# Performance work log

Measured on AMD Instinct MI355X. Metric: run time of the kernel, lower is better.

The kernel has to match this reference:

```python
import jax, jax.numpy as jnp
import numpy as np

M, K, N = 8192, 4096, 4096

def setup_inputs() -> dict:
    key = jax.random.key(0)
    k1, k2, k3, k4, k5, k6 = jax.random.split(key, 6)
    # quantized activations (per-token symmetric int8)
    x_q = jax.random.randint(k1, (M, K), -128, 128, dtype=jnp.int32).astype(jnp.int8)
    # quantized weight (asymmetric per-output-channel): w_fp16 = scale_weight * (w_q + zp_weight)
    weight = jax.random.randint(k2, (N, K), -128, 128, dtype=jnp.int32).astype(jnp.int8)
    scale_input = (jax.random.uniform(k3, (M,), jnp.float32) * 0.009 + 0.001).astype(jnp.float16)
    scale_weight = (jax.random.uniform(k4, (N,), jnp.float32) * 0.009 + 0.001).astype(jnp.float16)
    zp_weight = jax.random.randint(k5, (N,), 100, 156, dtype=jnp.int32).astype(jnp.int16)
    bias = (jax.random.normal(k6, (N,), jnp.float32) * 0.01).astype(jnp.float16)
    # per-row sum of quantized activations (needed for zero-point correction)
    sum_input = jnp.sum(x_q.astype(jnp.int32), axis=-1).astype(jnp.float32)
    return {
        "input": x_q,
        "weight": weight,
        "bias": bias,
        "scale_input": scale_input,
        "scale_weight": scale_weight,
        "sum_input": sum_input,
        "zp_weight": zp_weight,
    }

def reference(input, weight, bias, scale_input, scale_weight, sum_input, zp_weight):
    acc = jnp.matmul(input.astype(jnp.int32), weight.astype(jnp.int32).T)
    # asymmetric weight zero-point correction: + zp_n * sum_k(x_q[m, k])
    corr = sum_input[:, None] * zp_weight.astype(jnp.float32)[None, :]
    # fused dequant epilogue: per-row activation scale * per-col weight scale, + bias
    scale = scale_input.astype(jnp.float32)[:, None] * scale_weight.astype(jnp.float32)[None, :]
    out = (acc.astype(jnp.float32) + corr) * scale + bias.astype(jnp.float32)[None, :]
    return out.astype(jnp.float16)
```

## Files before the change

### kernel.cpp

```cpp
#include <hip/hip_runtime.h>
#include <stdint.h>


#define BM 128
#define BN 128
#define BK 128

typedef __attribute__((ext_vector_type(4))) int int32x4;
typedef __attribute__((ext_vector_type(16))) int int32x16;

__device__ __forceinline__ void async_copy16(const uint8_t* g, uint8_t* l) {
  __builtin_amdgcn_global_load_lds(
      (const __attribute__((address_space(1))) uint32_t*)(const void*)g,
      (__attribute__((address_space(3))) uint32_t*)l,
      16, 0, 0);
}

__global__ __launch_bounds__(256) void pack_kernel(
    const int* __restrict__ A, const int* __restrict__ B,
    uint8_t* __restrict__ A8, uint8_t* __restrict__ B8,
    int nA4, int nTot4) {
  const int stride = gridDim.x * blockDim.x;
  for (int t = blockIdx.x * blockDim.x + threadIdx.x; t < nTot4; t += stride) {
    const int32x4* src;
    uint32_t* dst;
    if (t < nA4) {
      src = (const int32x4*)A + t;
      dst = (uint32_t*)A8 + t;
    } else {
      int u = t - nA4;
      src = (const int32x4*)B + u;
      dst = (uint32_t*)B8 + u;
    }
    int32x4 v = __builtin_nontemporal_load(src);
    *dst = (uint32_t)(v.x & 255) | ((uint32_t)(v.y & 255) << 8) |
           ((uint32_t)(v.z & 255) << 16) | ((uint32_t)(v.w & 255) << 24);
  }
}

__device__ __forceinline__ void stage_tile(
    const uint8_t* Ab, const uint8_t* Bb, size_t sK, int k0,
    uint8_t* AsBuf, uint8_t* BsBuf, int ldst) {
#pragma unroll
  for (int p = 0; p < 4; ++p)
    async_copy16(Ab + (size_t)(p * 32) * sK + k0, AsBuf + p * 4096 + ldst);
#pragma unroll
  for (int p = 0; p < 4; ++p)
    async_copy16(Bb + (size_t)(p * 32) * sK + k0, BsBuf + p * 4096 + ldst);
}

__global__ __launch_bounds__(256, 2) void w8a8_gemm(
    const uint8_t* __restrict__ A8, const uint8_t* __restrict__ B8,
    const float* __restrict__ bias,
    const float* __restrict__ s_in,
    const float* __restrict__ s_w,
    const float* __restrict__ sum_in,
    const int* __restrict__ zp_w,
    float* __restrict__ out,
    int M, int N, int K) {
  __shared__ uint8_t As[2][BM * BK];
  __shared__ uint8_t Bs[2][BN * BK];

  const int tid = threadIdx.x;
  const int bm = blockIdx.y, bn = blockIdx.x;
  const int row0 = bm * BM, col0 = bn * BN;

  const int wave = tid >> 6, lane = tid & 63;
  const int m32 = lane & 31, half = lane >> 5;
  const int wm = (wave >> 1) * 64;
  const int wn = (wave & 1) * 64;
  const size_t sK = (size_t)K;

  const int row_s = tid >> 3;
  const int cg = (tid & 7) ^ ((tid >> 4) & 7);
  const int ldst = tid * 16;

  const uint8_t* Ab = A8 + (size_t)(row0 + row_s) * sK + cg * 16;
  const uint8_t* Bb = B8 + (size_t)(col0 + row_s) * sK + cg * 16;

  int32x16 acc[2][2] = {};

  const int NT = K / BK;
  stage_tile(Ab, Bb, sK, 0, &As[0][0], &Bs[0][0], ldst);
  stage_tile(Ab, Bb, sK, BK, &As[1][0], &Bs[1][0], ldst);

  int cur = 0;
  const int swzr = (m32 >> 1) & 7;
  for (int kt = 0; kt < NT; ++kt) {
    if (kt + 1 < NT) {
      asm volatile("s_waitcnt vmcnt(8)" ::: "memory");
    } else {
      asm volatile("s_waitcnt vmcnt(0)" ::: "memory");
    }
    __builtin_amdgcn_s_barrier();

    const uint8_t* Ac = &As[cur][0];
    const uint8_t* Bc = &Bs[cur][0];
#pragma unroll
    for (int ks = 0; ks < 4; ++ks) {
      const int gran = ((ks * 2 + half) ^ swzr) * 16;
      int32x4 afrag[2], bfrag[2];
#pragma unroll
      for (int i = 0; i < 2; ++i)
        afrag[i] = *(const int32x4*)&Ac[(wm + i * 32 + m32) * BK + gran];
#pragma unroll
      for (int j = 0; j < 2; ++j)
        bfrag[j] = *(const int32x4*)&Bc[(wn + j * 32 + m32) * BK + gran];
#pragma unroll
      for (int i = 0; i < 2; ++i)
#pragma unroll
        for (int j = 0; j < 2; ++j)
          acc[i][j] = __builtin_amdgcn_mfma_i32_32x32x32_i8(
              afrag[i], bfrag[j], acc[i][j], 0, 0, 0);
    }
    asm volatile("s_waitcnt lgkmcnt(0)" ::: "memory");
    __builtin_amdgcn_s_barrier();
    if (kt + 2 < NT)
      stage_tile(Ab, Bb, sK, (kt + 2) * BK, &As[cur][0], &Bs[cur][0], ldst);
    cur ^= 1;
  }

  float swj[2], zpj[2], bj[2];
#pragma unroll
  for (int j = 0; j < 2; ++j) {
    int gc = col0 + wn + j * 32 + m32;
    swj[j] = s_w[gc];
    zpj[j] = (float)zp_w[gc];
    bj[j] = bias[gc];
  }
#pragma unroll
  for (int i = 0; i < 2; ++i) {
#pragma unroll
    for (int reg = 0; reg < 16; ++reg) {
      int gr = row0 + wm + i * 32 + (reg & 3) + 8 * (reg >> 2) + 4 * half;
      float siv = s_in[gr];
      float suv = sum_in[gr];
      float* orow = out + (size_t)gr * N + col0 + wn + m32;
#pragma unroll
      for (int j = 0; j < 2; ++j) {
        float v = ((float)acc[i][j][reg] + suv * zpj[j]) * (siv * swj[j]) + bj[j];
        __builtin_nontemporal_store(v, &orow[j * 32]);
      }
    }
  }
}

__global__ __launch_bounds__(256) void w8a8_gemm_fallback(
    const int* __restrict__ A32, const int* __restrict__ B32,
    const float* __restrict__ bias,
    const float* __restrict__ s_in,
    const float* __restrict__ s_w,
    const float* __restrict__ sum_in,
    const int* __restrict__ zp_w,
    float* __restrict__ out,
    int M, int N, int K) {
  __shared__ uint8_t As[128 * 64];
  __shared__ uint8_t Bs[128 * 64];
  const int tid = threadIdx.x;
  const int bm = blockIdx.y, bn = blockIdx.x;
  const int row0 = bm * 128, col0 = bn * 128;
  const int wave = tid >> 6, lane = tid & 63;
  const int quad = lane >> 4, r = lane & 15;
  const int wm = (wave >> 1) * 64, wn = (wave & 1) * 64;
  const int lin = tid * 16;
  const int srow = lin >> 6;
  const int scol = lin & 63;
  const size_t sK = (size_t)K;
  int32x4 acc[4][4] = {};
  for (int k0 = 0; k0 < K; k0 += 64) {
#pragma unroll
    for (int c = 0; c < 2; ++c) {
      const int* ag = A32 + (size_t)(row0 + srow + c * 64) * sK + k0 + scol;
      const int* bg = B32 + (size_t)(col0 + srow + c * 64) * sK + k0 + scol;
      int32x4 pa, pb;
#pragma unroll
      for (int q = 0; q < 4; ++q) {
        int4 va = ((const int4*)ag)[q];
        int4 vb = ((const int4*)bg)[q];
        pa[q] = (int)((uint32_t)(va.x & 255) | ((uint32_t)(va.y & 255) << 8) |
                      ((uint32_t)(va.z & 255) << 16) | ((uint32_t)(va.w & 255) << 24));
        pb[q] = (int)((uint32_t)(vb.x & 255) | ((uint32_t)(vb.y & 255) << 8) |
                      ((uint32_t)(vb.z & 255) << 16) | ((uint32_t)(vb.w & 255) << 24));
      }
      *(int32x4*)&As[lin + c * 4096] = pa;
      *(int32x4*)&Bs[lin + c * 4096] = pb;
    }
    __syncthreads();
    int32x4 afrag[4], bfrag[4];
#pragma unroll
    for (int i = 0; i < 4; ++i)
      afrag[i] = *(const int32x4*)&As[(wm + i * 16 + r) * 64 + quad * 16];
#pragma unroll
    for (int j = 0; j < 4; ++j)
      bfrag[j] = *(const int32x4*)&Bs[(wn + j * 16 + r) * 64 + quad * 16];
#pragma unroll
    for (int i = 0; i < 4; ++i)
#pragma unroll
      for (int j = 0; j < 4; ++j)
        acc[i][j] = __builtin_amdgcn_mfma_i32_16x16x64_i8(afrag[i], bfrag[j],
                                                          acc[i][j], 0, 0, 0);
    __syncthreads();
  }
  float swj[4], zpj[4], bj[4];
#pragma unroll
  for (int j = 0; j < 4; ++j) {
    int gc = col0 + wn + j * 16 + r;
    swj[j] = s_w[gc];
    zpj[j] = (float)zp_w[gc];
    bj[j] = bias[gc];
  }
#pragma unroll
  for (int i = 0; i < 4; ++i) {
#pragma unroll
    for (int t = 0; t < 4; ++t) {
      int gr = row0 + wm + i * 16 + quad * 4 + t;
      float siv = s_in[gr];
      float suv = sum_in[gr];
      float* orow = out + (size_t)gr * N + col0 + wn + r;
#pragma unroll
      for (int j = 0; j < 4; ++j) {
        float v = ((float)acc[i][j][t] + suv * zpj[j]) * (siv * swj[j]) + bj[j];
        orow[j * 16] = v;
      }
    }
  }
}

extern "C" void kernel_launch(void* const* d_in, const int* in_sizes, int n_in,
                              void* d_out, int out_size, void* d_ws, size_t ws_size,
                              hipStream_t stream) {
  const int* x_q = (const int*)d_in[0];
  const int* w_q = (const int*)d_in[1];
  const float* bias = (const float*)d_in[2];
  const float* s_in = (const float*)d_in[3];
  const float* s_w = (const float*)d_in[4];
  const float* sum_in = (const float*)d_in[5];
  const int* zp_w = (const int*)d_in[6];
  float* out = (float*)d_out;

  const int M = in_sizes[3];
  const int N = in_sizes[2];
  const int K = in_sizes[0] / M;

  const size_t needA = (size_t)M * K;
  const size_t needB = (size_t)N * K;

  if (ws_size >= needA + needB && (M % BM) == 0 && (N % BN) == 0 &&
      (K % BK) == 0 && (K / BK) >= 2) {
    uint8_t* A8 = (uint8_t*)d_ws;
    uint8_t* B8 = A8 + needA;
    const int nA4 = (int)(needA / 4);
    const int nTot4 = (int)((needA + needB) / 4);
    int nblk = (nTot4 + 255) / 256;
    if (nblk > 2048) nblk = 2048;
    pack_kernel<<<nblk, 256, 0, stream>>>(x_q, w_q, A8, B8, nA4, nTot4);
    dim3 grid(N / BN, M / BM), block(256);
    w8a8_gemm<<<grid, block, 0, stream>>>(A8, B8, bias, s_in, s_w, sum_in,
                                          zp_w, out, M, N, K);
  } else {
    dim3 grid(N / 128, M / 128), block(256);
    w8a8_gemm_fallback<<<grid, block, 0, stream>>>(x_q, w_q, bias, s_in, s_w,
                                                   sum_in, zp_w, out, M, N, K);
  }
}
```

Baseline: 406.5 us.

## Replace double-buffered LDS pipeline with single buffer to raise occupancy

```diff
diff --git a/kernel.cpp b/kernel.cpp
--- a/kernel.cpp
+++ b/kernel.cpp
@@ -49,7 +49,7 @@
     async_copy16(Bb + (size_t)(p * 32) * sK + k0, BsBuf + p * 4096 + ldst);
 }
 
-__global__ __launch_bounds__(256, 2) void w8a8_gemm(
+__global__ __launch_bounds__(256, 4) void w8a8_gemm(
     const uint8_t* __restrict__ A8, const uint8_t* __restrict__ B8,
     const float* __restrict__ bias,
     const float* __restrict__ s_in,
@@ -58,8 +58,8 @@
     const int* __restrict__ zp_w,
     float* __restrict__ out,
     int M, int N, int K) {
-  __shared__ uint8_t As[2][BM * BK];
-  __shared__ uint8_t Bs[2][BN * BK];
+  __shared__ uint8_t As[BM * BK];
+  __shared__ uint8_t Bs[BN * BK];
 
   const int tid = threadIdx.x;
   const int bm = blockIdx.y, bn = blockIdx.x;
@@ -80,32 +80,21 @@
 
   int32x16 acc[2][2] = {};
 
-  const int NT = K / BK;
-  stage_tile(Ab, Bb, sK, 0, &As[0][0], &Bs[0][0], ldst);
-  stage_tile(Ab, Bb, sK, BK, &As[1][0], &Bs[1][0], ldst);
-
-  int cur = 0;
   const int swzr = (m32 >> 1) & 7;
-  for (int kt = 0; kt < NT; ++kt) {
-    if (kt + 1 < NT) {
-      asm volatile("s_waitcnt vmcnt(8)" ::: "memory");
-    } else {
-      asm volatile("s_waitcnt vmcnt(0)" ::: "memory");
-    }
-    __builtin_amdgcn_s_barrier();
-
-    const uint8_t* Ac = &As[cur][0];
-    const uint8_t* Bc = &Bs[cur][0];
+  for (int k0 = 0; k0 < K; k0 += BK) {
+    stage_tile(Ab, Bb, sK, k0, As, Bs, ldst);
+    __syncthreads();
+
 #pragma unroll
     for (int ks = 0; ks < 4; ++ks) {
       const int gran = ((ks * 2 + half) ^ swzr) * 16;
       int32x4 afrag[2], bfrag[2];
 #pragma unroll
       for (int i = 0; i < 2; ++i)
-        afrag[i] = *(const int32x4*)&Ac[(wm + i * 32 + m32) * BK + gran];
+        afrag[i] = *(const int32x4*)&As[(wm + i * 32 + m32) * BK + gran];
 #pragma unroll
       for (int j = 0; j < 2; ++j)
-        bfrag[j] = *(const int32x4*)&Bc[(wn + j * 32 + m32) * BK + gran];
+        bfrag[j] = *(const int32x4*)&Bs[(wn + j * 32 + m32) * BK + gran];
 #pragma unroll
       for (int i = 0; i < 2; ++i)
 #pragma unroll
@@ -113,11 +102,7 @@
           acc[i][j] = __builtin_amdgcn_mfma_i32_32x32x32_i8(
               afrag[i], bfrag[j], acc[i][j], 0, 0, 0);
     }
-    asm volatile("s_waitcnt lgkmcnt(0)" ::: "memory");
-    __builtin_amdgcn_s_barrier();
-    if (kt + 2 < NT)
-      stage_tile(Ab, Bb, sK, (kt + 2) * BK, &As[cur][0], &Bs[cur][0], ldst);
-    cur ^= 1;
+    __syncthreads();
   }
 
   float swj[2], zpj[2], bj[2];
@@ -246,7 +231,7 @@
   const size_t needB = (size_t)N * K;
 
   if (ws_size >= needA + needB && (M % BM) == 0 && (N % BN) == 0 &&
-      (K % BK) == 0 && (K / BK) >= 2) {
+      (K % BK) == 0) {
     uint8_t* A8 = (uint8_t*)d_ws;
     uint8_t* B8 = A8 + needA;
     const int nA4 = (int)(needA / 4);
```

After: 398.4 us. 2.0% less time.
